# Kernel optimization log

Hardware: AMD Instinct MI355X
Metric: run time of the kernel (lower is better)

Reference implementation:

```python
import jax, jax.numpy as jnp
import numpy as np

B, L, D = 128, 512, 768   # batch, bert tokens, bert hidden
J = 32                    # clause boundaries -> S = J + 1 segments
S = J + 1
DM, DF = 200, 200         # transformer d_model / ffn dim
EPS = 1e-5


def _ln(x, g, b):
    m = x.mean(-1, keepdims=True)
    v = ((x - m) ** 2).mean(-1, keepdims=True)
    return (x - m) / jnp.sqrt(v + EPS) * g + b


def setup_inputs() -> dict:
    key = jax.random.key(0)
    ks = jax.random.split(key, 12)
    sc = 0.02
    hidden_state = jax.random.normal(ks[0], (B, L, D), jnp.float32)
    # strictly increasing, positive clause boundaries < L (non-empty segments)
    seg = L // S  # stride ~= 15 tokens per clause
    jitter = jax.random.randint(ks[1], (B, J), 0, seg).astype(jnp.int32)
    clause_idx = jnp.arange(1, J + 1, dtype=jnp.int32)[None, :] * seg + jitter
    p = lambda k, shp: sc * jax.random.normal(k, shp, jnp.float32)
    z = lambda n: jnp.zeros((n,), jnp.float32)
    return {
        'hidden_state': hidden_state,
        'clause_idx': clause_idx,
        'fc5_w': p(ks[2], (1, D)), 'fc5_b': z(1),
        'fc1_w': p(ks[3], (DM, D)), 'fc1_b': z(DM),
        'attn_in_w': p(ks[4], (3 * DM, DM)), 'attn_in_b': z(3 * DM),
        'attn_out_w': p(ks[5], (DM, DM)), 'attn_out_b': z(DM),
        'ln1_g': jnp.ones((DM,), jnp.float32), 'ln1_b': z(DM),
        'lin1_w': p(ks[6], (DF, DM)), 'lin1_b': z(DF),
        'lin2_w': p(ks[7], (DM, DF)), 'lin2_b': z(DM),
        'ln2_g': jnp.ones((DM,), jnp.float32), 'ln2_b': z(DM),
        'fc_w': p(ks[8], (2, 2 * DM)), 'fc_b': z(2),
    }


def reference(hidden_state, clause_idx, fc5_w, fc5_b, fc1_w, fc1_b,
              attn_in_w, attn_in_b, attn_out_w, attn_out_b,
              ln1_g, ln1_b, lin1_w, lin1_b, lin2_w, lin2_b,
              ln2_g, ln2_b, fc_w, fc_b):
    # ---- ragged per-segment attention pooling (batched_index_select) ----
    t = jnp.arange(L)
    # segment id of each token: number of boundaries <= t  -> [B, L] in [0, S)
    seg_id = jnp.sum(t[None, None, :] >= clause_idx[:, :, None], axis=1)
    scores = jnp.einsum('bld,d->bl', hidden_state, fc5_w[0]) + fc5_b[0]  # fc5
    mask = seg_id[:, None, :] == jnp.arange(S)[None, :, None]            # [B,S,L]
    logits = jnp.where(mask, scores[:, None, :], -jnp.inf)
    w = jax.nn.softmax(logits, axis=-1)        # per-segment softmax over tokens
    pooled = jnp.einsum('bsl,bld->bsd', w, hidden_state)                 # [B,S,D]

    # ---- fc1 + TransformerEncoderLayer (post-norm, 1 head, relu, no dropout)
    x = pooled @ fc1_w.T + fc1_b                                         # [B,S,DM]
    qkv = x @ attn_in_w.T + attn_in_b
    q, k, v = jnp.split(qkv, 3, axis=-1)
    a = jax.nn.softmax(jnp.einsum('bqd,bkd->bqk', q, k) * (1.0 / np.sqrt(DM).item()), axis=-1)
    att = jnp.einsum('bqk,bkd->bqd', a, v) @ attn_out_w.T + attn_out_b
    x = _ln(x + att, ln1_g, ln1_b)
    ff = jax.nn.relu(x @ lin1_w.T + lin1_b) @ lin2_w.T + lin2_b
    x = _ln(x + ff, ln2_g, ln2_b)

    # ---- cat(first-token broadcast, rest) then classifier fc ----
    h = jnp.concatenate([jnp.broadcast_to(x[:, :1, :], (B, S - 1, DM)), x[:, 1:, :]], axis=-1)
    return h @ fc_w.T + fc_b                                             # [B, S-1, 2]
```

## Files before the change

### kernel.cpp

```cpp
#include <hip/hip_runtime.h>

#define NB 128
#define LL 512
#define DD 768
#define JJ 32
#define SS 33
#define DM 200

typedef __attribute__((ext_vector_type(8))) short bf8_t;
typedef __attribute__((ext_vector_type(4))) float f4_t;

#define SB_XF   0
#define SB_QB   61440
#define SB_KB   82944
#define SB_VT   104448
#define SB_Y2   235520
#define SB_BLK  275456

static __device__ __forceinline__ unsigned short f2bf(float f) {
  unsigned u = __float_as_uint(f);
  return (unsigned short)((u + 0x7FFFu + ((u >> 16) & 1u)) >> 16);
}

template<int KS>
static __device__ __forceinline__ f4_t mfma_tile(
    const unsigned short* pa, const unsigned short* pw)
{
  f4_t acc = {0.f, 0.f, 0.f, 0.f};
  bf8_t a = *(const bf8_t*)pa;
  bf8_t w = *(const bf8_t*)pw;
#pragma unroll
  for (int s = 1; s < KS; ++s) {
    bf8_t a2 = *(const bf8_t*)(pa + 32 * s);
    bf8_t w2 = *(const bf8_t*)(pw + 32 * s);
    acc = __builtin_amdgcn_mfma_f32_16x16x32_bf16(a, w, acc, 0, 0, 0);
    a = a2; w = w2;
  }
  acc = __builtin_amdgcn_mfma_f32_16x16x32_bf16(a, w, acc, 0, 0, 0);
  return acc;
}

template<int KS>
static __device__ __forceinline__ f4_t mfma_tile_lds(
    const unsigned short* pa, const unsigned short* pw)
{
  f4_t acc = {0.f, 0.f, 0.f, 0.f};
#pragma unroll
  for (int s = 0; s < KS; ++s) {
    bf8_t a = *(const bf8_t*)(pa + 32 * s);
    bf8_t w = *(const bf8_t*)(pw + 32 * s);
    acc = __builtin_amdgcn_mfma_f32_16x16x32_bf16(a, w, acc, 0, 0, 0);
  }
  return acc;
}

__global__ __launch_bounds__(512, 4) void pc_kernel(
    const float* __restrict__ hidden, const int* __restrict__ clause,
    const float* __restrict__ fc5w, unsigned short* __restrict__ pooled_bf,
    const float* __restrict__ fc1_w, const float* __restrict__ ain_w,
    const float* __restrict__ aout_w, const float* __restrict__ lin1_w,
    const float* __restrict__ lin2_w,
    unsigned short* __restrict__ fc1_wb, unsigned short* __restrict__ ain_wb,
    unsigned short* __restrict__ aout_wb, unsigned short* __restrict__ lin1_wb,
    unsigned short* __restrict__ lin2_wb, char* __restrict__ scratch)
{
  const int tid = threadIdx.x;
  if (blockIdx.x >= NB * SS) {
    int t = (blockIdx.x - NB * SS) * 512 + tid;
    if (t < 208 * 768) {
      int n = t / 768, k = t - n * 768;
      fc1_wb[t] = f2bf((n < 200) ? fc1_w[n * 768 + k] : 0.f);
      return;
    }
    t -= 208 * 768;
    if (t < 608 * 224) {
      int n = t / 224, k = t - n * 224;
      ain_wb[t] = f2bf((n < 600 && k < 200) ? ain_w[n * 200 + k] : 0.f);
      return;
    }
    t -= 608 * 224;
    if (t < 208 * 224) {
      int n = t / 224, k = t - n * 224;
      aout_wb[t] = f2bf((n < 200 && k < 200) ? aout_w[n * 200 + k] : 0.f);
      return;
    }
    t -= 208 * 224;
    if (t < 208 * 224) {
      int n = t / 224, k = t - n * 224;
      lin1_wb[t] = f2bf((n < 200 && k < 200) ? lin1_w[n * 200 + k] : 0.f);
      return;
    }
    t -= 208 * 224;
    if (t < 208 * 224) {
      int n = t / 224, k = t - n * 224;
      lin2_wb[t] = f2bf((n < 200 && k < 200) ? lin2_w[n * 200 + k] : 0.f);
      return;
    }
    t -= 208 * 224;
    if (t < NB * 1344) {
      int b = t / 1344, r = t - b * 1344;
      char* sb = scratch + (size_t)b * SB_BLK;
      const uint4 z = make_uint4(0, 0, 0, 0);
      if (r < 384) {
        int bi = r / 192, rr = r - bi * 192;
        int row = rr >> 2, c = rr & 3;
        int off = (bi == 0) ? SB_QB : SB_KB;
        *(uint4*)((unsigned short*)(sb + off) + row * 224 + 192 + c * 8) = z;
      } else {
        int rr = r - 384;
        int row = rr >> 2, c = rr & 3;
        *(uint4*)((unsigned short*)(sb + SB_VT) + row * 64 + 32 + c * 8) = z;
      }
    }
    return;
  }

  int blk = blockIdx.x;
  int b = blk / SS;
  int s = blk - b * SS;
  int t0 = (s == 0) ? 0 : clause[b * JJ + s - 1];
  int t1 = (s == JJ) ? LL : clause[b * JJ + s];
  int nt = t1 - t0;
  if (nt > 64) nt = 64;
  if (nt < 1) nt = 1;

  __shared__ float wsm[64];
  __shared__ __align__(16) float pw[8][772];
  int wave = tid >> 6, lane = tid & 63;

  const float4* w4 = (const float4*)fc5w;
  float4 wa = w4[lane], wwb = w4[lane + 64], wc = w4[lane + 128];

  float4 hv[4][3];
#pragma unroll
  for (int i = 0; i < 4; ++i) {
    int r = wave + 8 * i;
    if (r < nt) {
      const float4* hp = (const float4*)(hidden + ((long long)b * LL + t0 + r) * DD);
      float4 h0 = hp[lane], h1 = hp[lane + 64], h2 = hp[lane + 128];
      hv[i][0] = h0; hv[i][1] = h1; hv[i][2] = h2;
      float acc = h0.x*wa.x + h0.y*wa.y + h0.z*wa.z + h0.w*wa.w
                + h1.x*wwb.x + h1.y*wwb.y + h1.z*wwb.z + h1.w*wwb.w
                + h2.x*wc.x + h2.y*wc.y + h2.z*wc.z + h2.w*wc.w;
#pragma unroll
      for (int off = 32; off; off >>= 1) acc += __shfl_xor(acc, off);
      if (lane == 0) wsm[r] = acc;
    }
  }
  for (int r = wave + 32; r < nt; r += 8) {
    const float4* hp = (const float4*)(hidden + ((long long)b * LL + t0 + r) * DD);
    float4 h0 = hp[lane], h1 = hp[lane + 64], h2 = hp[lane + 128];
    float acc = h0.x*wa.x + h0.y*wa.y + h0.z*wa.z + h0.w*wa.w
              + h1.x*wwb.x + h1.y*wwb.y + h1.z*wwb.z + h1.w*wwb.w
              + h2.x*wc.x + h2.y*wc.y + h2.z*wc.z + h2.w*wc.w;
#pragma unroll
    for (int off = 32; off; off >>= 1) acc += __shfl_xor(acc, off);
    if (lane == 0) wsm[r] = acc;
  }
  __syncthreads();

  if (wave == 0) {
    float v = (lane < nt) ? wsm[lane] : -__builtin_inff();
    float mx = v;
#pragma unroll
    for (int off = 32; off; off >>= 1) mx = fmaxf(mx, __shfl_xor(mx, off));
    float e = (lane < nt) ? __expf(v - mx) : 0.f;
    float sm = e;
#pragma unroll
    for (int off = 32; off; off >>= 1) sm += __shfl_xor(sm, off);
    if (lane < nt) wsm[lane] = e / sm;
  }
  __syncthreads();

  float4 p0 = {0,0,0,0}, p1 = {0,0,0,0}, p2 = {0,0,0,0};
#pragma unroll
  for (int i = 0; i < 4; ++i) {
    int r = wave + 8 * i;
    if (r < nt) {
      float w = wsm[r];
      p0.x = fmaf(w, hv[i][0].x, p0.x); p0.y = fmaf(w, hv[i][0].y, p0.y);
      p0.z = fmaf(w, hv[i][0].z, p0.z); p0.w = fmaf(w, hv[i][0].w, p0.w);
      p1.x = fmaf(w, hv[i][1].x, p1.x); p1.y = fmaf(w, hv[i][1].y, p1.y);
      p1.z = fmaf(w, hv[i][1].z, p1.z); p1.w = fmaf(w, hv[i][1].w, p1.w);
      p2.x = fmaf(w, hv[i][2].x, p2.x); p2.y = fmaf(w, hv[i][2].y, p2.y);
      p2.z = fmaf(w, hv[i][2].z, p2.z); p2.w = fmaf(w, hv[i][2].w, p2.w);
    }
  }
  for (int r = wave + 32; r < nt; r += 8) {
    const float4* hp = (const float4*)(hidden + ((long long)b * LL + t0 + r) * DD);
    float w = wsm[r];
    float4 h0 = hp[lane], h1 = hp[lane + 64], h2 = hp[lane + 128];
    p0.x = fmaf(w, h0.x, p0.x); p0.y = fmaf(w, h0.y, p0.y);
    p0.z = fmaf(w, h0.z, p0.z); p0.w = fmaf(w, h0.w, p0.w);
    p1.x = fmaf(w, h1.x, p1.x); p1.y = fmaf(w, h1.y, p1.y);
    p1.z = fmaf(w, h1.z, p1.z); p1.w = fmaf(w, h1.w, p1.w);
    p2.x = fmaf(w, h2.x, p2.x); p2.y = fmaf(w, h2.y, p2.y);
    p2.z = fmaf(w, h2.z, p2.z); p2.w = fmaf(w, h2.w, p2.w);
  }
  {
    float4* pp = (float4*)&pw[wave][0];
    pp[lane] = p0; pp[lane + 64] = p1; pp[lane + 128] = p2;
  }
  __syncthreads();

  if (tid < 384) {
    float2 acc = make_float2(0.f, 0.f);
#pragma unroll
    for (int w = 0; w < 8; ++w) {
      float2 v = *(const float2*)&pw[w][tid * 2];
      acc.x += v.x; acc.y += v.y;
    }
    ushort2 o;
    o.x = f2bf(acc.x); o.y = f2bf(acc.y);
    *(ushort2*)(pooled_bf + (long long)blk * DD + tid * 2) = o;
  }
}

__global__ __launch_bounds__(512, 4) void k_fc1qkv(
    const unsigned short* __restrict__ pooled,
    const unsigned short* __restrict__ fc1_wb, const float* __restrict__ fc1_b,
    const unsigned short* __restrict__ ain_wb, const float* __restrict__ ain_b,
    char* __restrict__ scratch)
{
  const int b = blockIdx.x / 3, mt = blockIdx.x % 3, m0 = mt * 16;
  const int tid = threadIdx.x, wv = tid >> 6, lane = tid & 63;
  const int col = lane & 15, quad = lane >> 4, koff = quad * 8;

  char* sb = scratch + (size_t)b * SB_BLK;
  float* x_f32 = (float*)(sb + SB_XF);
  unsigned short* q_bf  = (unsigned short*)(sb + SB_QB);
  unsigned short* k_bf  = (unsigned short*)(sb + SB_KB);
  unsigned short* vt_bf = (unsigned short*)(sb + SB_VT);

  __shared__ __align__(16) unsigned short sA[16][776];
  __shared__ __align__(16) unsigned short xb[16][232];

  {
    int r = tid >> 5, c = tid & 31;
    int src = m0 + r; if (src > 32) src = 32;
    const unsigned* gp = (const unsigned*)(pooled + (size_t)(b * SS + src) * DD);
    unsigned* lp = (unsigned*)&sA[r][0];
#pragma unroll
    for (int i = 0; i < 12; ++i) lp[c + 32 * i] = gp[c + 32 * i];
  }
  for (int u = tid; u < 16 * 16; u += 512) {
    int row = u >> 4, c = u & 15;
    ((unsigned*)&xb[row][200])[c] = 0u;
  }
  __syncthreads();

  for (int t = wv; t < 13; t += 8) {
    int n0 = t * 16;
    f4_t acc = mfma_tile_lds<24>(&sA[0][0] + col * 776 + koff,
                                 fc1_wb + (size_t)(n0 + col) * DD + koff);
    int gn = n0 + col;
    if (gn < DM) {
      float bv = fc1_b[gn];
#pragma unroll
      for (int r = 0; r < 4; ++r) {
        int row = quad * 4 + r;
        float v = acc[r] + bv;
        x_f32[(m0 + row) * 208 + gn] = v;
        xb[row][gn] = f2bf(v);
      }
    }
  }
  __syncthreads();

  for (int t = wv; t < 38; t += 8) {
    int n0 = t * 16;
    f4_t acc = mfma_tile_lds<7>(&xb[0][0] + col * 232 + koff,
                                ain_wb + (size_t)(n0 + col) * 224 + koff);
    int gn = n0 + col;
    if (gn < 600) {
      float bv = ain_b[gn];
#pragma unroll
      for (int r = 0; r < 4; ++r) {
        int gm = m0 + quad * 4 + r;
        unsigned short bfv = f2bf(acc[r] + bv);
        if (gn < 200)      q_bf[gm * 224 + gn] = bfv;
        else if (gn < 400) k_bf[gm * 224 + (gn - 200)] = bfv;
        else if (gm < SS)  vt_bf[(gn - 400) * 64 + gm] = bfv;
      }
    }
  }
}

__global__ __launch_bounds__(512, 4) void k_postattn(
    const unsigned short* __restrict__ aout_wb, const float* __restrict__ aout_b,
    const float* __restrict__ ln1_g, const float* __restrict__ ln1_b,
    const unsigned short* __restrict__ lin1_wb, const float* __restrict__ lin1_b,
    const unsigned short* __restrict__ lin2_wb, const float* __restrict__ lin2_b,
    const float* __restrict__ ln2_g, const float* __restrict__ ln2_b,
    char* __restrict__ scratch)
{
  const int b = blockIdx.x / 3, mt = blockIdx.x % 3, m0 = mt * 16;
  const int tid = threadIdx.x, wv = tid >> 6, lane = tid & 63;
  const int col = lane & 15, quad = lane >> 4, koff = quad * 8;

  char* sb = scratch + (size_t)b * SB_BLK;
  const unsigned short* q_bf  = (const unsigned short*)(sb + SB_QB);
  const unsigned short* k_bf  = (const unsigned short*)(sb + SB_KB);
  const unsigned short* vt_bf = (const unsigned short*)(sb + SB_VT);
  const float* x_f32 = (const float*)(sb + SB_XF);
  float* y2g = (float*)(sb + SB_Y2);

  __shared__ float tc[16][211];
  __shared__ __align__(16) unsigned short Pb[16][72];
  __shared__ __align__(16) unsigned short yb[16][232];
  __shared__ __align__(16) unsigned short fb[16][232];
  for (int u = tid; u < 16 * 16; u += 512) {
    int row = u >> 4, c = u & 15;
    ((unsigned*)&yb[row][200])[c] = 0u;
    ((unsigned*)&fb[row][200])[c] = 0u;
  }

  for (int t = wv; t < 3; t += 8) {
    int n0 = t * 16;
    f4_t acc = mfma_tile<7>(q_bf + (m0 + col) * 224 + koff,
                            k_bf + (n0 + col) * 224 + koff);
    int gn = n0 + col;
#pragma unroll
    for (int r = 0; r < 4; ++r)
      tc[quad * 4 + r][gn] = acc[r] * 0.07071067811865475f;
  }
  __syncthreads();

  for (int r = wv; r < 16; r += 8) {
    bool live = (m0 + r) < SS;
    float v = (lane < SS && live) ? tc[r][lane] : -__builtin_inff();
    float mx = v;
#pragma unroll
    for (int off = 32; off; off >>= 1) mx = fmaxf(mx, __shfl_xor(mx, off));
    float e = (lane < SS && live) ? __expf(v - mx) : 0.f;
    float sm = e;
#pragma unroll
    for (int off = 32; off; off >>= 1) sm += __shfl_xor(sm, off);
    Pb[r][lane] = (lane < SS && live) ? f2bf(e / sm) : (unsigned short)0;
  }
  __syncthreads();

  for (int t = wv; t < 13; t += 8) {
    int n0 = t * 16;
    f4_t acc = mfma_tile_lds<2>(&Pb[0][0] + col * 72 + koff,
                                vt_bf + (n0 + col) * 64 + koff);
    int gn = n0 + col;
    if (gn < DM) {
#pragma unroll
      for (int r = 0; r < 4; ++r)
        fb[quad * 4 + r][gn] = f2bf(acc[r]);
    }
  }
  __syncthreads();

  for (int t = wv; t < 13; t += 8) {
    int n0 = t * 16;
    f4_t acc = mfma_tile_lds<7>(&fb[0][0] + col * 232 + koff,
                                aout_wb + (size_t)(n0 + col) * 224 + koff);
    int gn = n0 + col;
    float bv = (gn < DM) ? aout_b[gn] : 0.f;
#pragma unroll
    for (int r = 0; r < 4; ++r) {
      int row = quad * 4 + r;
      float v = acc[r] + bv;
      if (gn < DM) v += x_f32[(m0 + row) * 208 + gn];
      tc[row][gn] = v;
    }
  }
  __syncthreads();

  for (int r = wv; r < 16; r += 8) {
    float* p = &tc[r][0];
    float vals[4]; float s = 0.f;
#pragma unroll
    for (int i = 0; i < 4; ++i) { int k = lane + 64 * i; vals[i] = (k < DM) ? p[k] : 0.f; s += vals[i]; }
#pragma unroll
    for (int off = 32; off; off >>= 1) s += __shfl_xor(s, off);
    float mean = s * (1.f / DM);
    float vs = 0.f;
#pragma unroll
    for (int i = 0; i < 4; ++i) { int k = lane + 64 * i; if (k < DM) { float d = vals[i] - mean; vs += d * d; } }
#pragma unroll
    for (int off = 32; off; off >>= 1) vs += __shfl_xor(vs, off);
    float rstd = rsqrtf(vs * (1.f / DM) + 1e-5f);
#pragma unroll
    for (int i = 0; i < 4; ++i) {
      int k = lane + 64 * i;
      if (k < DM) {
        float o = (vals[i] - mean) * rstd * ln1_g[k] + ln1_b[k];
        p[k] = o;
        yb[r][k] = f2bf(o);
      }
    }
  }
  __syncthreads();

  for (int t = wv; t < 13; t += 8) {
    int n0 = t * 16;
    f4_t acc = mfma_tile_lds<7>(&yb[0][0] + col * 232 + koff,
                                lin1_wb + (size_t)(n0 + col) * 224 + koff);
    int gn = n0 + col;
    if (gn < DM) {
      float bv = lin1_b[gn];
#pragma unroll
      for (int r = 0; r < 4; ++r)
        fb[quad * 4 + r][gn] = f2bf(fmaxf(acc[r] + bv, 0.f));
    }
  }
  __syncthreads();

  for (int t = wv; t < 13; t += 8) {
    int n0 = t * 16;
    f4_t acc = mfma_tile_lds<7>(&fb[0][0] + col * 232 + koff,
                                lin2_wb + (size_t)(n0 + col) * 224 + koff);
    int gn = n0 + col;
    if (gn < DM) {
      float bv = lin2_b[gn];
#pragma unroll
      for (int r = 0; r < 4; ++r) {
        int row = quad * 4 + r;
        tc[row][gn] = acc[r] + bv + tc[row][gn];
      }
    }
  }
  __syncthreads();

  for (int r = wv; r < 16; r += 8) {
    float* p = &tc[r][0];
    float vals[4]; float s = 0.f;
#pragma unroll
    for (int i = 0; i < 4; ++i) { int k = lane + 64 * i; vals[i] = (k < DM) ? p[k] : 0.f; s += vals[i]; }
#pragma unroll
    for (int off = 32; off; off >>= 1) s += __shfl_xor(s, off);
    float mean = s * (1.f / DM);
    float vs = 0.f;
#pragma unroll
    for (int i = 0; i < 4; ++i) { int k = lane + 64 * i; if (k < DM) { float d = vals[i] - mean; vs += d * d; } }
#pragma unroll
    for (int off = 32; off; off >>= 1) vs += __shfl_xor(vs, off);
    float rstd = rsqrtf(vs * (1.f / DM) + 1e-5f);
    int grow = m0 + r;
#pragma unroll
    for (int i = 0; i < 4; ++i) {
      int k = lane + 64 * i;
      if (k < DM) y2g[grow * 208 + k] = (vals[i] - mean) * rstd * ln2_g[k] + ln2_b[k];
    }
  }
}

__global__ __launch_bounds__(256) void k_cls(
    const char* __restrict__ scratch, const float* __restrict__ fcw,
    const float* __restrict__ fcb, float* __restrict__ out)
{
  int gw = blockIdx.x * 4 + (threadIdx.x >> 6);
  int lane = threadIdx.x & 63;
  int b = gw >> 5, j = gw & 31;
  const float* y2 = (const float*)(scratch + (size_t)b * SB_BLK + SB_Y2);
  const float* r0 = y2;
  const float* rj = y2 + (1 + j) * 208;
  float a0 = 0.f, a1 = 0.f;
  for (int k = lane; k < DM; k += 64) {
    float u = r0[k], w = rj[k];
    a0 += u * fcw[k]       + w * fcw[200 + k];
    a1 += u * fcw[400 + k] + w * fcw[600 + k];
  }
#pragma unroll
  for (int off = 32; off; off >>= 1) {
    a0 += __shfl_xor(a0, off);
    a1 += __shfl_xor(a1, off);
  }
  if (lane == 0) {
    out[gw * 2 + 0] = a0 + fcb[0];
    out[gw * 2 + 1] = a1 + fcb[1];
  }
}

extern "C" void kernel_launch(void* const* d_in, const int* in_sizes, int n_in,
                              void* d_out, int out_size, void* d_ws, size_t ws_size,
                              hipStream_t stream)
{
  (void)in_sizes; (void)n_in; (void)out_size; (void)ws_size;
  const float* hidden = (const float*)d_in[0];
  const int*   clause = (const int*)d_in[1];
  const float* fc5_w  = (const float*)d_in[2];
  const float* fc1_w  = (const float*)d_in[4];
  const float* fc1_b  = (const float*)d_in[5];
  const float* ain_w  = (const float*)d_in[6];
  const float* ain_b  = (const float*)d_in[7];
  const float* aout_w = (const float*)d_in[8];
  const float* aout_b = (const float*)d_in[9];
  const float* ln1_g  = (const float*)d_in[10];
  const float* ln1_b  = (const float*)d_in[11];
  const float* lin1_w = (const float*)d_in[12];
  const float* lin1_b = (const float*)d_in[13];
  const float* lin2_w = (const float*)d_in[14];
  const float* lin2_b = (const float*)d_in[15];
  const float* ln2_g  = (const float*)d_in[16];
  const float* ln2_b  = (const float*)d_in[17];
  const float* fc_w   = (const float*)d_in[18];
  const float* fc_b   = (const float*)d_in[19];
  float* out = (float*)d_out;

  char* w8 = (char*)d_ws;
  unsigned short* pooled_bf = (unsigned short*)(w8 + 0);
  char* scratch = w8 + 6520832;
  size_t wbase = 6520832 + (size_t)NB * SB_BLK;
  unsigned short* fc1_wb  = (unsigned short*)(w8 + wbase);
  unsigned short* ain_wb  = (unsigned short*)(w8 + wbase + 319488);
  unsigned short* aout_wb = (unsigned short*)(w8 + wbase + 591872);
  unsigned short* lin1_wb = (unsigned short*)(w8 + wbase + 685056);
  unsigned short* lin2_wb = (unsigned short*)(w8 + wbase + 778240);

  pc_kernel<<<dim3(NB * SS + 1187), 512, 0, stream>>>(
      hidden, clause, fc5_w, pooled_bf,
      fc1_w, ain_w, aout_w, lin1_w, lin2_w,
      fc1_wb, ain_wb, aout_wb, lin1_wb, lin2_wb, scratch);
  k_fc1qkv<<<dim3(NB * 3), 512, 0, stream>>>(pooled_bf, fc1_wb, fc1_b,
      ain_wb, ain_b, scratch);
  k_postattn<<<dim3(NB * 3), 512, 0, stream>>>(aout_wb, aout_b, ln1_g, ln1_b,
      lin1_wb, lin1_b, lin2_wb, lin2_b, ln2_g, ln2_b, scratch);
  k_cls<<<dim3(1024), 256, 0, stream>>>(scratch, fc_w, fc_b, out);
}
```

Measured before the change: 367.6 us.

## Fuse classifier into post-attention kernel via atomic accumulation, drop k_cls launch

Removes the separate classifier kernel: k_postattn now keeps the LN2 output in shared memory and computes each row's classifier contribution, atomically adding it into the output. The output is zeroed in k_fc1qkv, and the y2 scratch region is dropped, shrinking the per-batch scratch stride. The hidden-state loads in the pooling kernel are also split from the dot-product math so more loads are in flight at once. This saves one launch and a global round trip, at the cost of float atomics and order-dependent summation.

```diff
diff --git a/kernel.cpp b/kernel.cpp
--- a/kernel.cpp
+++ b/kernel.cpp
@@ -14,8 +14,7 @@
 #define SB_QB   61440
 #define SB_KB   82944
 #define SB_VT   104448
-#define SB_Y2   235520
-#define SB_BLK  275456
+#define SB_BLK  131072
 
 static __device__ __forceinline__ unsigned short f2bf(float f) {
   unsigned u = __float_as_uint(f);
@@ -109,7 +108,8 @@
       } else {
         int rr = r - 384;
         int row = rr >> 2, c = rr & 3;
-        *(uint4*)((unsigned short*)(sb + SB_VT) + row * 64 + 32 + c * 8) = z;
+        if (row < 208)
+          *(uint4*)((unsigned short*)(sb + SB_VT) + row * 64 + 32 + c * 8) = z;
       }
     }
     return;
@@ -137,8 +137,14 @@
     int r = wave + 8 * i;
     if (r < nt) {
       const float4* hp = (const float4*)(hidden + ((long long)b * LL + t0 + r) * DD);
-      float4 h0 = hp[lane], h1 = hp[lane + 64], h2 = hp[lane + 128];
-      hv[i][0] = h0; hv[i][1] = h1; hv[i][2] = h2;
+      hv[i][0] = hp[lane]; hv[i][1] = hp[lane + 64]; hv[i][2] = hp[lane + 128];
+    }
+  }
+#pragma unroll
+  for (int i = 0; i < 4; ++i) {
+    int r = wave + 8 * i;
+    if (r < nt) {
+      float4 h0 = hv[i][0], h1 = hv[i][1], h2 = hv[i][2];
       float acc = h0.x*wa.x + h0.y*wa.y + h0.z*wa.z + h0.w*wa.w
                 + h1.x*wwb.x + h1.y*wwb.y + h1.z*wwb.z + h1.w*wwb.w
                 + h2.x*wc.x + h2.y*wc.y + h2.z*wc.z + h2.w*wc.w;
@@ -220,11 +226,13 @@
     const unsigned short* __restrict__ pooled,
     const unsigned short* __restrict__ fc1_wb, const float* __restrict__ fc1_b,
     const unsigned short* __restrict__ ain_wb, const float* __restrict__ ain_b,
-    char* __restrict__ scratch)
+    char* __restrict__ scratch, float* __restrict__ out)
 {
   const int b = blockIdx.x / 3, mt = blockIdx.x % 3, m0 = mt * 16;
   const int tid = threadIdx.x, wv = tid >> 6, lane = tid & 63;
   const int col = lane & 15, quad = lane >> 4, koff = quad * 8;
+
+  if (blockIdx.x < 16) out[blockIdx.x * 512 + tid] = 0.f;
 
   char* sb = scratch + (size_t)b * SB_BLK;
   float* x_f32 = (float*)(sb + SB_XF);
@@ -292,7 +300,8 @@
     const unsigned short* __restrict__ lin1_wb, const float* __restrict__ lin1_b,
     const unsigned short* __restrict__ lin2_wb, const float* __restrict__ lin2_b,
     const float* __restrict__ ln2_g, const float* __restrict__ ln2_b,
-    char* __restrict__ scratch)
+    const float* __restrict__ fcw, const float* __restrict__ fcb,
+    char* __restrict__ scratch, float* __restrict__ out)
 {
   const int b = blockIdx.x / 3, mt = blockIdx.x % 3, m0 = mt * 16;
   const int tid = threadIdx.x, wv = tid >> 6, lane = tid & 63;
@@ -303,7 +312,6 @@
   const unsigned short* k_bf  = (const unsigned short*)(sb + SB_KB);
   const unsigned short* vt_bf = (const unsigned short*)(sb + SB_VT);
   const float* x_f32 = (const float*)(sb + SB_XF);
-  float* y2g = (float*)(sb + SB_Y2);
 
   __shared__ float tc[16][211];
   __shared__ __align__(16) unsigned short Pb[16][72];
@@ -439,39 +447,52 @@
 #pragma unroll
     for (int off = 32; off; off >>= 1) vs += __shfl_xor(vs, off);
     float rstd = rsqrtf(vs * (1.f / DM) + 1e-5f);
-    int grow = m0 + r;
 #pragma unroll
     for (int i = 0; i < 4; ++i) {
       int k = lane + 64 * i;
-      if (k < DM) y2g[grow * 208 + k] = (vals[i] - mean) * rstd * ln2_g[k] + ln2_b[k];
-    }
-  }
-}
-
-__global__ __launch_bounds__(256) void k_cls(
-    const char* __restrict__ scratch, const float* __restrict__ fcw,
-    const float* __restrict__ fcb, float* __restrict__ out)
-{
-  int gw = blockIdx.x * 4 + (threadIdx.x >> 6);
-  int lane = threadIdx.x & 63;
-  int b = gw >> 5, j = gw & 31;
-  const float* y2 = (const float*)(scratch + (size_t)b * SB_BLK + SB_Y2);
-  const float* r0 = y2;
-  const float* rj = y2 + (1 + j) * 208;
-  float a0 = 0.f, a1 = 0.f;
-  for (int k = lane; k < DM; k += 64) {
-    float u = r0[k], w = rj[k];
-    a0 += u * fcw[k]       + w * fcw[200 + k];
-    a1 += u * fcw[400 + k] + w * fcw[600 + k];
-  }
-#pragma unroll
-  for (int off = 32; off; off >>= 1) {
-    a0 += __shfl_xor(a0, off);
-    a1 += __shfl_xor(a1, off);
-  }
-  if (lane == 0) {
-    out[gw * 2 + 0] = a0 + fcb[0];
-    out[gw * 2 + 1] = a1 + fcb[1];
+      if (k < DM) p[k] = (vals[i] - mean) * rstd * ln2_g[k] + ln2_b[k];
+    }
+  }
+  __syncthreads();
+
+  for (int r = wv; r < 16; r += 8) {
+    int grow = m0 + r;
+    if (grow >= SS) continue;
+    const float* p = &tc[r][0];
+    if (grow == 0) {
+      float s0 = 0.f, s1 = 0.f;
+#pragma unroll
+      for (int i = 0; i < 4; ++i) {
+        int k = lane + 64 * i;
+        if (k < DM) { float v = p[k]; s0 += v * fcw[k]; s1 += v * fcw[400 + k]; }
+      }
+#pragma unroll
+      for (int off = 32; off; off >>= 1) {
+        s0 += __shfl_xor(s0, off);
+        s1 += __shfl_xor(s1, off);
+      }
+      if (lane < 32) {
+        atomicAdd(&out[(b * 32 + lane) * 2 + 0], s0 + fcb[0]);
+        atomicAdd(&out[(b * 32 + lane) * 2 + 1], s1 + fcb[1]);
+      }
+    } else {
+      int j = grow - 1;
+      float a0 = 0.f, a1 = 0.f;
+#pragma unroll
+      for (int i = 0; i < 4; ++i) {
+        int k = lane + 64 * i;
+        if (k < DM) { float v = p[k]; a0 += v * fcw[200 + k]; a1 += v * fcw[600 + k]; }
+      }
+#pragma unroll
+      for (int off = 32; off; off >>= 1) {
+        a0 += __shfl_xor(a0, off);
+        a1 += __shfl_xor(a1, off);
+      }
+      if (lane == 0) {
+        atomicAdd(&out[(b * 32 + j) * 2 + 0], a0);
+        atomicAdd(&out[(b * 32 + j) * 2 + 1], a1);
+      }
+    }
   }
 }
 
@@ -516,8 +537,8 @@
       fc1_w, ain_w, aout_w, lin1_w, lin2_w,
       fc1_wb, ain_wb, aout_wb, lin1_wb, lin2_wb, scratch);
   k_fc1qkv<<<dim3(NB * 3), 512, 0, stream>>>(pooled_bf, fc1_wb, fc1_b,
-      ain_wb, ain_b, scratch);
+      ain_wb, ain_b, scratch, out);
   k_postattn<<<dim3(NB * 3), 512, 0, stream>>>(aout_wb, aout_b, ln1_g, ln1_b,
-      lin1_wb, lin1_b, lin2_wb, lin2_b, ln2_g, ln2_b, scratch);
-  k_cls<<<dim3(1024), 256, 0, stream>>>(scratch, fc_w, fc_b, out);
-}
+      lin1_wb, lin1_b, lin2_wb, lin2_b, ln2_g, ln2_b, fc_w, fc_b,
+      scratch, out);
+}
```

Measured after the change: 360.9 us. Within noise of the previous version (-1.8%).
